# Optimization experiments

Hardware: AMD Instinct MI355X
Metric: run time of the kernel (lower is better)

## Reference

```python
import jax, jax.numpy as jnp
import numpy as np

B, D = 2048, 256

def setup_inputs() -> dict:
    key = jax.random.key(0)
    ka, kb, kc, kh, ky, kl, ku = jax.random.split(key, 7)
    y = jax.random.normal(ky, (B, D), dtype=jnp.float32)
    # bounds bracketing y with random slack so the in-bounds mask is nontrivial
    l = y - 2.0 * jax.random.uniform(kl, (B, D), dtype=jnp.float32)
    u = y + 2.0 * jax.random.uniform(ku, (B, D), dtype=jnp.float32)
    a = jax.random.normal(ka, (B, D), dtype=jnp.float32)
    b = jax.random.normal(kb, (B, D), dtype=jnp.float32)
    c = jax.random.normal(kc, (B, D), dtype=jnp.float32)
    h = jax.random.normal(kh, (B, D), dtype=jnp.float32)
    return {"a": a, "b": b, "c": c, "l": l, "u": u, "h": h, "y": y}

def reference(a, b, c, l, u, h, y):
    # y: [B, D]; neighbors differ from y by +/-1 in exactly one coordinate
    d = y.shape[-1]
    e = jnp.eye(d, dtype=y.dtype)               # [D, D]
    yb = y[:, None, :]                           # [B, 1, D]
    n = jnp.concatenate([yb + e, yb - e], axis=-2)  # [B, 2D, D]
    lb = l[:, None, :]
    ub = u[:, None, :]
    nmsk = jnp.all((lb <= n) & (n <= ub), axis=-1)   # [B, 2D]
    return (n, nmsk)
```

## Files before the change

### kernel.cpp

```cpp
#include <hip/hip_runtime.h>


#define BB 2048
#define DD 256

__global__ __launch_bounds__(256) void nnns_kernel(
    const float* __restrict__ l,
    const float* __restrict__ u,
    const float* __restrict__ y,
    float* __restrict__ n_out,
    float* __restrict__ m_out)
{
    const int i   = blockIdx.x;
    const int tid = threadIdx.x;

    __shared__ int s_fail;
    if (tid == 0) s_fail = 0;
    __syncthreads();

    const int k = tid;
    const float yv = y[i * DD + k];
    const float lv = l[i * DD + k];
    const float uv = u[i * DD + k];
    const bool ok = (lv <= yv) && (yv <= uv);
    if (!ok) atomicAdd(&s_fail, 1);
    __syncthreads();
    const int fail = s_fail;

    const bool others = (fail == 0) || (fail == 1 && !ok);
    const float yp = yv + 1.0f;
    const float ym = yv - 1.0f;
    const bool okp = (lv <= yp) && (yp <= uv);
    const bool okm = (lv <= ym) && (ym <= uv);
    m_out[(size_t)i * (2 * DD) + k]      = (others && okp) ? 1.0f : 0.0f;
    m_out[(size_t)i * (2 * DD) + DD + k] = (others && okm) ? 1.0f : 0.0f;

    const int lane = tid & 63;
    const int jg   = tid >> 6;
    const int kb   = lane * 4;

    const float4 y4 = *(const float4*)(y + i * DD + kb);
    float4* nrow = (float4*)(n_out + (size_t)i * (2 * DD) * DD);

    #pragma unroll 4
    for (int j0 = 0; j0 < 2 * DD; j0 += 4) {
        const int j = j0 + jg;
        float4 v;
        v.x = y4.x + ((j == kb + 0) ? 1.0f : 0.0f) - ((j == kb + DD + 0) ? 1.0f : 0.0f);
        v.y = y4.y + ((j == kb + 1) ? 1.0f : 0.0f) - ((j == kb + DD + 1) ? 1.0f : 0.0f);
        v.z = y4.z + ((j == kb + 2) ? 1.0f : 0.0f) - ((j == kb + DD + 2) ? 1.0f : 0.0f);
        v.w = y4.w + ((j == kb + 3) ? 1.0f : 0.0f) - ((j == kb + DD + 3) ? 1.0f : 0.0f);
        nrow[(size_t)j * (DD / 4) + lane] = v;
    }
}

extern "C" void kernel_launch(void* const* d_in, const int* in_sizes, int n_in,
                              void* d_out, int out_size, void* d_ws, size_t ws_size,
                              hipStream_t stream) {
    const float* l = (const float*)d_in[3];
    const float* u = (const float*)d_in[4];
    const float* y = (const float*)d_in[6];

    float* n_out = (float*)d_out;
    float* m_out = (float*)d_out + (size_t)BB * (2 * DD) * DD;

    nnns_kernel<<<dim3(BB), dim3(256), 0, stream>>>(l, u, y, n_out, m_out);
}
```

Before: 1.050 ms.

## Assign one wavefront per batch row and use nontemporal stores for neighbors

Each 64-lane wavefront now owns a whole batch row, so a block covers four rows and the grid shrinks to a quarter. The LDS atomic count and both block barriers are replaced by a wave-level shuffle reduction, and the mask is written with vector stores. The large neighbor tensor is written through nontemporal stores with simpler per-element index arithmetic, to cut cache pollution and ALU work on a write-bound kernel. The trade-off is that each wave now issues all 512 row stores itself.

Result: no change. 1.061 ms (+1.1%).

```diff
diff --git a/kernel.cpp b/kernel.cpp
--- a/kernel.cpp
+++ b/kernel.cpp
@@ -3,6 +3,8 @@
 
 #define BB 2048
 #define DD 256
+
+typedef float v4f __attribute__((ext_vector_type(4)));
 
 __global__ __launch_bounds__(256) void nnns_kernel(
     const float* __restrict__ l,
@@ -11,46 +13,55 @@
     float* __restrict__ n_out,
     float* __restrict__ m_out)
 {
-    const int i   = blockIdx.x;
-    const int tid = threadIdx.x;
-
-    __shared__ int s_fail;
-    if (tid == 0) s_fail = 0;
-    __syncthreads();
-
-    const int k = tid;
-    const float yv = y[i * DD + k];
-    const float lv = l[i * DD + k];
-    const float uv = u[i * DD + k];
-    const bool ok = (lv <= yv) && (yv <= uv);
-    if (!ok) atomicAdd(&s_fail, 1);
-    __syncthreads();
-    const int fail = s_fail;
-
-    const bool others = (fail == 0) || (fail == 1 && !ok);
-    const float yp = yv + 1.0f;
-    const float ym = yv - 1.0f;
-    const bool okp = (lv <= yp) && (yp <= uv);
-    const bool okm = (lv <= ym) && (ym <= uv);
-    m_out[(size_t)i * (2 * DD) + k]      = (others && okp) ? 1.0f : 0.0f;
-    m_out[(size_t)i * (2 * DD) + DD + k] = (others && okm) ? 1.0f : 0.0f;
-
-    const int lane = tid & 63;
-    const int jg   = tid >> 6;
+    const int lane = threadIdx.x & 63;
+    const int w    = threadIdx.x >> 6;
+    const int i    = blockIdx.x * 4 + w;
     const int kb   = lane * 4;
 
-    const float4 y4 = *(const float4*)(y + i * DD + kb);
-    float4* nrow = (float4*)(n_out + (size_t)i * (2 * DD) * DD);
+    const v4f y4 = *(const v4f*)(y + i * DD + kb);
+    const v4f l4 = *(const v4f*)(l + i * DD + kb);
+    const v4f u4 = *(const v4f*)(u + i * DD + kb);
+
+    const int c0 = (l4.x <= y4.x) && (y4.x <= u4.x);
+    const int c1 = (l4.y <= y4.y) && (y4.y <= u4.y);
+    const int c2 = (l4.z <= y4.z) && (y4.z <= u4.z);
+    const int c3 = (l4.w <= y4.w) && (y4.w <= u4.w);
+    int f = 4 - (c0 + c1 + c2 + c3);
+    #pragma unroll
+    for (int off = 32; off; off >>= 1) f += __shfl_xor(f, off);
+
+    const float mp0 = ((f == 0) || (f == 1 && !c0)) && (l4.x <= y4.x + 1.0f) && (y4.x + 1.0f <= u4.x);
+    const float mp1 = ((f == 0) || (f == 1 && !c1)) && (l4.y <= y4.y + 1.0f) && (y4.y + 1.0f <= u4.y);
+    const float mp2 = ((f == 0) || (f == 1 && !c2)) && (l4.z <= y4.z + 1.0f) && (y4.z + 1.0f <= u4.z);
+    const float mp3 = ((f == 0) || (f == 1 && !c3)) && (l4.w <= y4.w + 1.0f) && (y4.w + 1.0f <= u4.w);
+    const float mm0 = ((f == 0) || (f == 1 && !c0)) && (l4.x <= y4.x - 1.0f) && (y4.x - 1.0f <= u4.x);
+    const float mm1 = ((f == 0) || (f == 1 && !c1)) && (l4.y <= y4.y - 1.0f) && (y4.y - 1.0f <= u4.y);
+    const float mm2 = ((f == 0) || (f == 1 && !c2)) && (l4.z <= y4.z - 1.0f) && (y4.z - 1.0f <= u4.z);
+    const float mm3 = ((f == 0) || (f == 1 && !c3)) && (l4.w <= y4.w - 1.0f) && (y4.w - 1.0f <= u4.w);
+    v4f mp = {mp0, mp1, mp2, mp3};
+    v4f mm = {mm0, mm1, mm2, mm3};
+    *(v4f*)(m_out + (size_t)i * (2 * DD) + kb)      = mp;
+    *(v4f*)(m_out + (size_t)i * (2 * DD) + DD + kb) = mm;
+
+    v4f* p = (v4f*)(n_out + (size_t)i * (2 * DD) * DD) + lane;
 
     #pragma unroll 4
-    for (int j0 = 0; j0 < 2 * DD; j0 += 4) {
-        const int j = j0 + jg;
-        float4 v;
-        v.x = y4.x + ((j == kb + 0) ? 1.0f : 0.0f) - ((j == kb + DD + 0) ? 1.0f : 0.0f);
-        v.y = y4.y + ((j == kb + 1) ? 1.0f : 0.0f) - ((j == kb + DD + 1) ? 1.0f : 0.0f);
-        v.z = y4.z + ((j == kb + 2) ? 1.0f : 0.0f) - ((j == kb + DD + 2) ? 1.0f : 0.0f);
-        v.w = y4.w + ((j == kb + 3) ? 1.0f : 0.0f) - ((j == kb + DD + 3) ? 1.0f : 0.0f);
-        nrow[(size_t)j * (DD / 4) + lane] = v;
+    for (int t4 = 0; t4 < DD; t4 += 4) {
+        const int tl = t4 >> 2;
+        v4f v;
+        v = y4; v.x += (lane == tl) ? 1.0f : 0.0f; __builtin_nontemporal_store(v, p); p += 64;
+        v = y4; v.y += (lane == tl) ? 1.0f : 0.0f; __builtin_nontemporal_store(v, p); p += 64;
+        v = y4; v.z += (lane == tl) ? 1.0f : 0.0f; __builtin_nontemporal_store(v, p); p += 64;
+        v = y4; v.w += (lane == tl) ? 1.0f : 0.0f; __builtin_nontemporal_store(v, p); p += 64;
+    }
+    #pragma unroll 4
+    for (int t4 = 0; t4 < DD; t4 += 4) {
+        const int tl = t4 >> 2;
+        v4f v;
+        v = y4; v.x -= (lane == tl) ? 1.0f : 0.0f; __builtin_nontemporal_store(v, p); p += 64;
+        v = y4; v.y -= (lane == tl) ? 1.0f : 0.0f; __builtin_nontemporal_store(v, p); p += 64;
+        v = y4; v.z -= (lane == tl) ? 1.0f : 0.0f; __builtin_nontemporal_store(v, p); p += 64;
+        v = y4; v.w -= (lane == tl) ? 1.0f : 0.0f; __builtin_nontemporal_store(v, p); p += 64;
     }
 }
 
@@ -64,5 +75,5 @@
     float* n_out = (float*)d_out;
     float* m_out = (float*)d_out + (size_t)BB * (2 * DD) * DD;
 
-    nnns_kernel<<<dim3(BB), dim3(256), 0, stream>>>(l, u, y, n_out, m_out);
+    nnns_kernel<<<dim3(BB / 4), dim3(256), 0, stream>>>(l, u, y, n_out, m_out);
 }
```
